# Kernel optimization log

Measured on AMD Instinct MI355X. Metric: run time of the kernel, lower is better.

Reference implementation:

```python
import jax, jax.numpy as jnp
import numpy as np

B, L, D, H, M = 2, 1024, 1024, 16, 64
DH = D // H  # depth per head


def setup_inputs() -> dict:
    key = jax.random.key(0)
    ks = jax.random.split(key, 7)
    s = 0.02
    return {
        "x": jax.random.normal(ks[0], (B, L, D), jnp.float32),
        "Wq": jax.random.normal(ks[1], (D, D), jnp.float32) * s,
        "Wk": jax.random.normal(ks[2], (D, D), jnp.float32) * s,
        "Wv": jax.random.normal(ks[3], (D, D), jnp.float32) * s,
        "Wo": jax.random.normal(ks[4], (D, D), jnp.float32) * s,
        "rel_k_table": jax.random.normal(ks[5], (2 * M + 1, DH), jnp.float32) * s,
        "rel_v_table": jax.random.normal(ks[6], (2 * M + 1, DH), jnp.float32) * s,
    }


def _rel_idx(length, max_rel):
    # Shaw-style clipped relative position indices: [L, L] in [0, 2*max_rel]
    r = jnp.arange(length)
    return jnp.clip(r[None, :] - r[:, None], -max_rel, max_rel) + max_rel


def _split_heads(t):
    # [B, L, D] -> [B, H, L, DH]
    return t.reshape(B, L, H, DH).transpose(0, 2, 1, 3)


def reference(x, Wq, Wk, Wv, Wo, rel_k_table, rel_v_table):
    q = _split_heads(x @ Wq) * (DH ** -0.5)  # T2T scales q by d_head^-0.5
    k = _split_heads(x @ Wk)
    v = _split_heads(x @ Wv)

    idx = _rel_idx(L, M)
    rel_k = rel_k_table[idx]  # [L, L, DH] gathered keys-relative embeddings
    rel_v = rel_v_table[idx]  # [L, L, DH]

    # _relative_attention_inner(q, k, rel_k, transpose=True)
    logits = jnp.einsum('bhid,bhjd->bhij', q, k) + jnp.einsum('bhid,ijd->bhij', q, rel_k)
    w = jax.nn.softmax(logits, axis=-1)  # [B, H, L, L]; dropout_rate=0 / inference

    # _relative_attention_inner(w, v, rel_v, transpose=False)
    o = jnp.einsum('bhij,bhjd->bhid', w, v) + jnp.einsum('bhij,ijd->bhid', w, rel_v)

    # combine heads then output transform
    o = o.transpose(0, 2, 1, 3).reshape(B, L, D)
    return o @ Wo
```

## Files before the change

kernel.cpp:

```cpp
#include <hip/hip_runtime.h>
#include <hip/hip_bf16.h>
#include <math.h>

#define B_ 2
#define L_ 1024
#define D_ 1024
#define H_ 16
#define DH_ 64
#define M_ 64
#define R_ 129
#define NLD ((size_t)B_ * L_ * D_)
#define DD  ((size_t)D_ * D_)
#define QSCALE 0.18033688011112042f

using bf16x8 = __attribute__((ext_vector_type(8))) short;
using f32x4  = __attribute__((ext_vector_type(4))) float;

__device__ __forceinline__ unsigned short f2bf(float f) {
    unsigned int x = __builtin_bit_cast(unsigned int, f);
    unsigned int r = x + 0x7fffu + ((x >> 16) & 1u);
    return (unsigned short)(r >> 16);
}
__device__ __forceinline__ float bf2f(unsigned short u) {
    unsigned int x = ((unsigned int)u) << 16;
    return __builtin_bit_cast(float, x);
}
__device__ __forceinline__ unsigned int pk2bf(float lo, float hi) {
    return (unsigned int)f2bf(lo) | ((unsigned int)f2bf(hi) << 16);
}

__global__ __launch_bounds__(256)
void prep(const float* __restrict__ x,
          const float* __restrict__ W0, const float* __restrict__ W1,
          const float* __restrict__ W2, const float* __restrict__ W3,
          const float* __restrict__ relk, const float* __restrict__ relv,
          unsigned short* __restrict__ xb, unsigned short* __restrict__ Wt,
          unsigned short* __restrict__ relkb, unsigned short* __restrict__ relvT)
{
    __shared__ float tile[32][33];
    const int bid = blockIdx.x, t = threadIdx.x;
    if (bid < 2048) {
        const int i = bid * 256 + t;
        float4 v = ((const float4*)x)[i];
        short4 o = { (short)f2bf(v.x), (short)f2bf(v.y), (short)f2bf(v.z), (short)f2bf(v.w) };
        ((short4*)xb)[i] = o;
    } else if (bid < 6144) {
        const int wb = bid - 2048;
        const int z = wb >> 10, rem = wb & 1023;
        const float* W = z == 0 ? W0 : z == 1 ? W1 : z == 2 ? W2 : W3;
        unsigned short* T = Wt + (size_t)z * DD;
        const int k0 = (rem >> 5) * 32, n0 = (rem & 31) * 32;
        const int r = t >> 3, c = (t & 7) * 4;
        float4 v = *(const float4*)&W[(size_t)(k0 + r) * D_ + n0 + c];
        tile[r][c] = v.x; tile[r][c + 1] = v.y; tile[r][c + 2] = v.z; tile[r][c + 3] = v.w;
        __syncthreads();
        short4 o = { (short)f2bf(tile[c][r]),     (short)f2bf(tile[c + 1][r]),
                     (short)f2bf(tile[c + 2][r]), (short)f2bf(tile[c + 3][r]) };
        *(short4*)&T[(size_t)(n0 + r) * D_ + k0 + c] = o;
    } else {
        const int idx = (bid - 6144) * 256 + t;
        if (idx < 144 * 64) {
            const int r = idx >> 6, d = idx & 63;
            relkb[idx] = (r < R_) ? f2bf(relk[r * 64 + d]) : (unsigned short)0;
        }
        if (idx < 64 * 136) {
            const int d = idx / 136, r = idx - d * 136;
            relvT[idx] = (r < R_) ? f2bf(relv[r * 64 + d]) : (unsigned short)0;
        }
    }
}

__global__ __launch_bounds__(256)
void gemm128(const unsigned short* __restrict__ A, const unsigned short* __restrict__ Bt,
             unsigned short* __restrict__ Cb, float* __restrict__ Cf, float scale0)
{
    __shared__ unsigned short As[128][64];
    __shared__ unsigned short Bs[128][64];

    const int t = threadIdx.x, lane = t & 63, wid = t >> 6;
    const int fr = lane & 15, g = lane >> 4;
    const int m0 = blockIdx.y * 128;
    const int nglob = blockIdx.x * 128;
    const int mat = nglob >> 10;
    const int n0 = nglob & 1023;
    const float scale = (mat == 0) ? scale0 : 1.f;
    const int wm = (wid >> 1) * 64, wn = (wid & 1) * 64;

    f32x4 acc[4][4] = {};

    int srow[4], skof[4], sdst[4];
#pragma unroll
    for (int c = 0; c < 4; ++c) {
        const int chunk = c * 256 + t;
        srow[c] = chunk >> 3;
        skof[c] = ((chunk & 7) ^ (srow[c] & 7)) * 8;
        sdst[c] = chunk * 8;
    }

    const unsigned short* Abase = A  + (size_t)m0 * D_;
    const unsigned short* Bbase = Bt + (size_t)nglob * D_;

    for (int k0 = 0; k0 < D_; k0 += 64) {
        __syncthreads();
#pragma unroll
        for (int c = 0; c < 4; ++c) {
            __builtin_amdgcn_global_load_lds(
                (const __attribute__((address_space(1))) void*)(Abase + (size_t)srow[c] * D_ + k0 + skof[c]),
                (__attribute__((address_space(3))) void*)(&As[0][0] + sdst[c]), 16, 0, 0);
            __builtin_amdgcn_global_load_lds(
                (const __attribute__((address_space(1))) void*)(Bbase + (size_t)srow[c] * D_ + k0 + skof[c]),
                (__attribute__((address_space(3))) void*)(&Bs[0][0] + sdst[c]), 16, 0, 0);
        }
        __syncthreads();

#pragma unroll
        for (int kb = 0; kb < 2; ++kb) {
            bf16x8 av[4], bv[4];
#pragma unroll
            for (int i = 0; i < 4; ++i) {
                const int ra = wm + i * 16 + fr;
                av[i] = *(const bf16x8*)&As[ra][(((kb << 2) + g) ^ (ra & 7)) * 8];
                const int rb = wn + i * 16 + fr;
                bv[i] = *(const bf16x8*)&Bs[rb][(((kb << 2) + g) ^ (rb & 7)) * 8];
            }
#pragma unroll
            for (int i = 0; i < 4; ++i)
#pragma unroll
                for (int j = 0; j < 4; ++j)
                    acc[i][j] = __builtin_amdgcn_mfma_f32_16x16x32_bf16(av[i], bv[j], acc[i][j], 0, 0, 0);
        }
    }

    const int orow = g * 4;
    if (Cb) {
        unsigned short* Cp = Cb + (size_t)mat * NLD;
#pragma unroll
        for (int i = 0; i < 4; ++i)
#pragma unroll
            for (int j = 0; j < 4; ++j) {
                unsigned short* cp = Cp + (size_t)(m0 + wm + i * 16 + orow) * D_ + n0 + wn + j * 16 + fr;
#pragma unroll
                for (int rg = 0; rg < 4; ++rg)
                    cp[(size_t)rg * D_] = f2bf(acc[i][j][rg] * scale);
            }
    } else {
#pragma unroll
        for (int i = 0; i < 4; ++i)
#pragma unroll
            for (int j = 0; j < 4; ++j) {
                float* cp = Cf + (size_t)(m0 + wm + i * 16 + orow) * D_ + n0 + wn + j * 16 + fr;
#pragma unroll
                for (int rg = 0; rg < 4; ++rg)
                    cp[(size_t)rg * D_] = acc[i][j][rg] * scale;
            }
    }
}

__device__ __forceinline__ void stage_k(const unsigned short* src, unsigned short* dst, int t)
{
#pragma unroll
    for (int it = 0; it < 2; ++it) {
        const int c = it * 256 + t;
        const int j = c >> 3;
        const int sc = (c & 7) ^ (j & 7);
        __builtin_amdgcn_global_load_lds(
            (const __attribute__((address_space(1))) void*)(src + (size_t)j * D_ + sc * 8),
            (__attribute__((address_space(3))) void*)(dst + c * 8), 16, 0, 0);
    }
}

__device__ __forceinline__ void write_vt(unsigned short (*Vtl)[64], int jp, int d0, bf16x8 a, bf16x8 b)
{
    const int jlo = (2 * jp) & 7;
    const int jc  = jp >> 2;
#pragma unroll
    for (int e = 0; e < 8; ++e) {
        const int d = d0 + e;
        const unsigned int val = (unsigned int)(unsigned short)a[e]
                               | ((unsigned int)(unsigned short)b[e] << 16);
        *(unsigned int*)&Vtl[d][((jc ^ (d & 7)) << 3) + jlo] = val;
    }
}

__global__ __launch_bounds__(256)
void attn_mfma(const unsigned short* __restrict__ Qb, const unsigned short* __restrict__ Kb,
               const unsigned short* __restrict__ Vb,
               const unsigned short* __restrict__ relkb,
               const unsigned short* __restrict__ relvT,
               const float* __restrict__ relv,
               unsigned short* __restrict__ Ob)
{
    __shared__ unsigned short Klds[2][64][64];
    __shared__ unsigned short Vt[2][64][64];
    __shared__ unsigned short Plds[64][72];
    __shared__ unsigned short QRs[64][136];
    __shared__ unsigned short Wsum[64][136];

    const int t    = threadIdx.x;
    const int lane = t & 63;
    const int w    = t >> 6;
    const int fr   = lane & 15;
    const int g    = lane >> 4;

    const int bx  = blockIdx.x;
    const int xcd = bx & 7, slot = bx >> 3;
    const int bh  = (xcd << 2) | (slot >> 4);
    const int rb  = slot & 15;
    const int b   = bh >> 4, h = bh & 15;
    const int i0  = rb * 64;
    const size_t head = (size_t)b * L_ * D_ + (size_t)h * DH_;

    const int iloc = w * 16 + fr;

    const unsigned short* Kh = Kb + head;
    const unsigned short* Vh = Vb + head;

    stage_k(Kh, &Klds[0][0][0], t);

    const int jp = t & 31, d0v = ((t >> 5) & 7) * 8;
    bf16x8 va  = *(const bf16x8*)(Vh + (size_t)(2 * jp) * D_ + d0v);
    bf16x8 vb2 = *(const bf16x8*)(Vh + (size_t)(2 * jp + 1) * D_ + d0v);

    {
        unsigned int* wp = (unsigned int*)&Wsum[0][0];
        for (int i = t; i < 64 * 136 / 2; i += 256) wp[i] = 0u;
    }

    bf16x8 qf[2];
    {
        const unsigned short* qp = Qb + head + (size_t)(i0 + iloc) * D_;
        qf[0] = *(const bf16x8*)(qp + g * 8);
        qf[1] = *(const bf16x8*)(qp + 32 + g * 8);
    }

#pragma unroll
    for (int rc = 0; rc < 9; ++rc) {
        f32x4 acc = {};
#pragma unroll
        for (int kb = 0; kb < 2; ++kb) {
            bf16x8 rv = *(const bf16x8*)&relkb[(size_t)(rc * 16 + fr) * 64 + kb * 32 + g * 8];
            acc = __builtin_amdgcn_mfma_f32_16x16x32_bf16(rv, qf[kb], acc, 0, 0, 0);
        }
        if (rc < 8) {
            uint2 pk = { pk2bf(acc[0], acc[1]), pk2bf(acc[2], acc[3]) };
            *(uint2*)&QRs[iloc][rc * 16 + g * 4] = pk;
        } else if (g == 0) {
            QRs[iloc][128] = f2bf(acc[0]);
        }
    }

    write_vt(Vt[0], jp, d0v, va, vb2);
    asm volatile("s_waitcnt vmcnt(0)" ::: "memory");
    __syncthreads();

    const float qr0   = bf2f(QRs[iloc][0]);
    const float qr128 = bf2f(QRs[iloc][128]);

    f32x4 oacc[4] = {};
    float lpart = 0.f, pe0p = 0.f, pe128p = 0.f;

    int bb = 0;
    for (int jt = 0; jt < 16; ++jt) {
        const bool pre = (jt < 15);
        if (pre) {
            stage_k(Kh + (size_t)(jt + 1) * 64 * D_, &Klds[bb ^ 1][0][0], t);
            const unsigned short* vp = Vh + (size_t)((jt + 1) * 64 + 2 * jp) * D_ + d0v;
            va  = *(const bf16x8*)vp;
            vb2 = *(const bf16x8*)(vp + D_);
        }

        f32x4 s[4];
        __builtin_amdgcn_s_setprio(1);
#pragma unroll
        for (int fc = 0; fc < 4; ++fc) {
            f32x4 a = {};
            const int j = fc * 16 + fr;
#pragma unroll
            for (int kb = 0; kb < 2; ++kb) {
                bf16x8 kv = *(const bf16x8*)&Klds[bb][j][(((kb << 2) + g) ^ (j & 7)) * 8];
                a = __builtin_amdgcn_mfma_f32_16x16x32_bf16(kv, qf[kb], a, 0, 0, 0);
            }
            s[fc] = a;
        }
        __builtin_amdgcn_s_setprio(0);

        const int dt   = (jt - rb) * 64;
        const int relb = dt - iloc + g * 4;

        if (dt <= -128 || dt >= 128) {
            const float qrc = (dt < 0) ? qr0 : qr128;
            float tsum = 0.f;
#pragma unroll
            for (int fc = 0; fc < 4; ++fc) {
                float p0 = exp2f(s[fc][0] + qrc);
                float p1 = exp2f(s[fc][1] + qrc);
                float p2 = exp2f(s[fc][2] + qrc);
                float p3 = exp2f(s[fc][3] + qrc);
                uint2 pk = { pk2bf(p0, p1), pk2bf(p2, p3) };
                *(uint2*)&Plds[iloc][fc * 16 + g * 4] = pk;
                tsum += (p0 + p1) + (p2 + p3);
            }
            lpart += tsum;
            if (dt < 0) pe0p += tsum; else pe128p += tsum;
        } else if (dt == 0) {
#pragma unroll
            for (int fc = 0; fc < 4; ++fc) {
                const int c0 = relb + fc * 16 + M_;
                float pe[4];
#pragma unroll
                for (int reg = 0; reg < 4; ++reg) {
                    pe[reg] = exp2f(s[fc][reg] + bf2f(QRs[iloc][c0 + reg]));
                    lpart += pe[reg];
                }
                uint2 pk = { pk2bf(pe[0], pe[1]), pk2bf(pe[2], pe[3]) };
                *(uint2*)&Plds[iloc][fc * 16 + g * 4] = pk;
                Wsum[iloc][c0 + 0] = (unsigned short)(pk.x & 0xffffu);
                Wsum[iloc][c0 + 1] = (unsigned short)(pk.x >> 16);
                Wsum[iloc][c0 + 2] = (unsigned short)(pk.y & 0xffffu);
                Wsum[iloc][c0 + 3] = (unsigned short)(pk.y >> 16);
            }
        } else {
#pragma unroll
            for (int fc = 0; fc < 4; ++fc) {
                float pe[4];
#pragma unroll
                for (int reg = 0; reg < 4; ++reg) {
                    const int colr = relb + fc * 16 + reg + M_;
                    const int col  = colr < 0 ? 0 : (colr > 128 ? 128 : colr);
                    pe[reg] = exp2f(s[fc][reg] + bf2f(QRs[iloc][col]));
                    lpart += pe[reg];
                    if (col == 0)        pe0p   += pe[reg];
                    else if (col == 128) pe128p += pe[reg];
                    else                 Wsum[iloc][col] = f2bf(pe[reg]);
                }
                uint2 pk = { pk2bf(pe[0], pe[1]), pk2bf(pe[2], pe[3]) };
                *(uint2*)&Plds[iloc][fc * 16 + g * 4] = pk;
            }
        }

        asm volatile("s_waitcnt lgkmcnt(0)" ::: "memory");
        __builtin_amdgcn_sched_barrier(0);

        bf16x8 pa0 = *(const bf16x8*)&Plds[iloc][g * 8];
        bf16x8 pa1 = *(const bf16x8*)&Plds[iloc][32 + g * 8];
        __builtin_amdgcn_s_setprio(1);
#pragma unroll
        for (int fd = 0; fd < 4; ++fd) {
            const int d = fd * 16 + fr;
            bf16x8 vv0 = *(const bf16x8*)&Vt[bb][d][((g)     ^ (d & 7)) * 8];
            bf16x8 vv1 = *(const bf16x8*)&Vt[bb][d][((4 + g) ^ (d & 7)) * 8];
            oacc[fd] = __builtin_amdgcn_mfma_f32_16x16x32_bf16(pa0, vv0, oacc[fd], 0, 0, 0);
            oacc[fd] = __builtin_amdgcn_mfma_f32_16x16x32_bf16(pa1, vv1, oacc[fd], 0, 0, 0);
        }
        __builtin_amdgcn_s_setprio(0);

        if (pre) write_vt(Vt[bb ^ 1], jp, d0v, va, vb2);
        asm volatile("s_waitcnt vmcnt(0)" ::: "memory");
        __syncthreads();
        bb ^= 1;
    }

    lpart  += __shfl_xor(lpart, 16);  lpart  += __shfl_xor(lpart, 32);
    pe0p   += __shfl_xor(pe0p, 16);   pe0p   += __shfl_xor(pe0p, 32);
    pe128p += __shfl_xor(pe128p, 16); pe128p += __shfl_xor(pe128p, 32);
    if (g == 0) {
        Wsum[iloc][0]   = f2bf(pe0p);
        Wsum[iloc][128] = f2bf(pe128p);
    }
    asm volatile("s_waitcnt lgkmcnt(0)" ::: "memory");
    __builtin_amdgcn_sched_barrier(0);

#pragma unroll
    for (int kc = 0; kc < 4; ++kc) {
        bf16x8 wa = *(const bf16x8*)&Wsum[iloc][kc * 32 + g * 8];
#pragma unroll
        for (int fd = 0; fd < 4; ++fd) {
            bf16x8 rv = *(const bf16x8*)&relvT[(size_t)(fd * 16 + fr) * 136 + kc * 32 + g * 8];
            oacc[fd] = __builtin_amdgcn_mfma_f32_16x16x32_bf16(wa, rv, oacc[fd], 0, 0, 0);
        }
    }

    float invd[4], pr128[4];
#pragma unroll
    for (int reg = 0; reg < 4; ++reg) {
        const int src = (lane & 48) | (g * 4 + reg);
        invd[reg]  = 1.f / __shfl(lpart, src, 64);
        pr128[reg] = __shfl(pe128p, src, 64);
    }

#pragma unroll
    for (int fd = 0; fd < 4; ++fd) {
        const float r128 = relv[128 * 64 + fd * 16 + fr];
        unsigned short* op = Ob + head + (size_t)(i0 + w * 16 + g * 4) * D_ + fd * 16 + fr;
#pragma unroll
        for (int reg = 0; reg < 4; ++reg)
            op[(size_t)reg * D_] = f2bf((oacc[fd][reg] + pr128[reg] * r128) * invd[reg]);
    }
}

extern "C" void kernel_launch(void* const* d_in, const int* in_sizes, int n_in,
                              void* d_out, int out_size, void* d_ws, size_t ws_size,
                              hipStream_t stream)
{
    const float* x    = (const float*)d_in[0];
    const float* Wq   = (const float*)d_in[1];
    const float* Wk   = (const float*)d_in[2];
    const float* Wv   = (const float*)d_in[3];
    const float* Wo   = (const float*)d_in[4];
    const float* relk = (const float*)d_in[5];
    const float* relv = (const float*)d_in[6];
    float* out = (float*)d_out;

    unsigned short* xb    = (unsigned short*)d_ws;
    unsigned short* Wt    = xb + NLD;
    unsigned short* relkb = Wt + 4 * DD;
    unsigned short* relvT = relkb + 144 * 64;
    unsigned short* QKVb  = relvT + 64 * 136;
    unsigned short* Ob    = QKVb + 3 * NLD;

    prep<<<dim3(6180), 256, 0, stream>>>(x, Wq, Wk, Wv, Wo, relk, relv, xb, Wt, relkb, relvT);

    gemm128<<<dim3(24, 16), 256, 0, stream>>>(xb, Wt, QKVb, nullptr, QSCALE);

    attn_mfma<<<dim3(512), 256, 0, stream>>>(QKVb, QKVb + NLD, QKVb + 2 * NLD,
                                             relkb, relvT, relv, Ob);

    gemm128<<<dim3(8, 16), 256, 0, stream>>>(Ob, Wt + 3 * DD, nullptr, out, 1.f);
}
```

Before: 91.63 us.

## Shrink GEMM M-tile to 64, hoist V loads in attention, use intrinsic bf16 pack

The projection GEMMs now use a 64x128 tile, so the QKV GEMM runs 768 blocks and the output GEMM 256 blocks. That gives more parallelism on the many CUs, at the price of less reuse of each B tile. In the attention kernel, the V fragment LDS reads are moved ahead of the softmax section so their latency overlaps the exp work, which costs extra registers. The manual float-to-bf16 pair packing is replaced with the HIP __float22bfloat162_rn intrinsic, which may map to a packed convert instruction.

```diff
diff --git a/kernel.cpp b/kernel.cpp
--- a/kernel.cpp
+++ b/kernel.cpp
@@ -26,7 +26,10 @@
     return __builtin_bit_cast(float, x);
 }
 __device__ __forceinline__ unsigned int pk2bf(float lo, float hi) {
-    return (unsigned int)f2bf(lo) | ((unsigned int)f2bf(hi) << 16);
+    __hip_bfloat162 h = __float22bfloat162_rn(float2{lo, hi});
+    unsigned int u;
+    __builtin_memcpy(&u, &h, 4);
+    return u;
 }
 
 __global__ __launch_bounds__(256)
@@ -71,30 +74,38 @@
 }
 
 __global__ __launch_bounds__(256)
-void gemm128(const unsigned short* __restrict__ A, const unsigned short* __restrict__ Bt,
-             unsigned short* __restrict__ Cb, float* __restrict__ Cf, float scale0)
-{
-    __shared__ unsigned short As[128][64];
+void gemm64(const unsigned short* __restrict__ A, const unsigned short* __restrict__ Bt,
+            unsigned short* __restrict__ Cb, float* __restrict__ Cf, float scale0)
+{
+    __shared__ unsigned short As[64][64];
     __shared__ unsigned short Bs[128][64];
 
     const int t = threadIdx.x, lane = t & 63, wid = t >> 6;
     const int fr = lane & 15, g = lane >> 4;
-    const int m0 = blockIdx.y * 128;
+    const int m0 = blockIdx.y * 64;
     const int nglob = blockIdx.x * 128;
     const int mat = nglob >> 10;
     const int n0 = nglob & 1023;
     const float scale = (mat == 0) ? scale0 : 1.f;
-    const int wm = (wid >> 1) * 64, wn = (wid & 1) * 64;
-
-    f32x4 acc[4][4] = {};
-
-    int srow[4], skof[4], sdst[4];
+    const int wm = (wid >> 1) * 32, wn = (wid & 1) * 64;
+
+    f32x4 acc[2][4] = {};
+
+    int arow[2], akof[2], adst[2];
+#pragma unroll
+    for (int c = 0; c < 2; ++c) {
+        const int chunk = c * 256 + t;
+        arow[c] = chunk >> 3;
+        akof[c] = ((chunk & 7) ^ (arow[c] & 7)) * 8;
+        adst[c] = chunk * 8;
+    }
+    int brow[4], bkof[4], bdst[4];
 #pragma unroll
     for (int c = 0; c < 4; ++c) {
         const int chunk = c * 256 + t;
-        srow[c] = chunk >> 3;
-        skof[c] = ((chunk & 7) ^ (srow[c] & 7)) * 8;
-        sdst[c] = chunk * 8;
+        brow[c] = chunk >> 3;
+        bkof[c] = ((chunk & 7) ^ (brow[c] & 7)) * 8;
+        bdst[c] = chunk * 8;
     }
 
     const unsigned short* Abase = A  + (size_t)m0 * D_;
@@ -103,28 +114,32 @@
     for (int k0 = 0; k0 < D_; k0 += 64) {
         __syncthreads();
 #pragma unroll
-        for (int c = 0; c < 4; ++c) {
+        for (int c = 0; c < 2; ++c)
             __builtin_amdgcn_global_load_lds(
-                (const __attribute__((address_space(1))) void*)(Abase + (size_t)srow[c] * D_ + k0 + skof[c]),
-                (__attribute__((address_space(3))) void*)(&As[0][0] + sdst[c]), 16, 0, 0);
+                (const __attribute__((address_space(1))) void*)(Abase + (size_t)arow[c] * D_ + k0 + akof[c]),
+                (__attribute__((address_space(3))) void*)(&As[0][0] + adst[c]), 16, 0, 0);
+#pragma unroll
+        for (int c = 0; c < 4; ++c)
             __builtin_amdgcn_global_load_lds(
-                (const __attribute__((address_space(1))) void*)(Bbase + (size_t)srow[c] * D_ + k0 + skof[c]),
-                (__attribute__((address_space(3))) void*)(&Bs[0][0] + sdst[c]), 16, 0, 0);
-        }
+                (const __attribute__((address_space(1))) void*)(Bbase + (size_t)brow[c] * D_ + k0 + bkof[c]),
+                (__attribute__((address_space(3))) void*)(&Bs[0][0] + bdst[c]), 16, 0, 0);
         __syncthreads();
 
 #pragma unroll
         for (int kb = 0; kb < 2; ++kb) {
-            bf16x8 av[4], bv[4];
-#pragma unroll
-            for (int i = 0; i < 4; ++i) {
+            bf16x8 av[2], bv[4];
+#pragma unroll
+            for (int i = 0; i < 2; ++i) {
                 const int ra = wm + i * 16 + fr;
                 av[i] = *(const bf16x8*)&As[ra][(((kb << 2) + g) ^ (ra & 7)) * 8];
-                const int rb = wn + i * 16 + fr;
-                bv[i] = *(const bf16x8*)&Bs[rb][(((kb << 2) + g) ^ (rb & 7)) * 8];
-            }
-#pragma unroll
-            for (int i = 0; i < 4; ++i)
+            }
+#pragma unroll
+            for (int j = 0; j < 4; ++j) {
+                const int rb = wn + j * 16 + fr;
+                bv[j] = *(const bf16x8*)&Bs[rb][(((kb << 2) + g) ^ (rb & 7)) * 8];
+            }
+#pragma unroll
+            for (int i = 0; i < 2; ++i)
 #pragma unroll
                 for (int j = 0; j < 4; ++j)
                     acc[i][j] = __builtin_amdgcn_mfma_f32_16x16x32_bf16(av[i], bv[j], acc[i][j], 0, 0, 0);
@@ -135,7 +150,7 @@
     if (Cb) {
         unsigned short* Cp = Cb + (size_t)mat * NLD;
 #pragma unroll
-        for (int i = 0; i < 4; ++i)
+        for (int i = 0; i < 2; ++i)
 #pragma unroll
             for (int j = 0; j < 4; ++j) {
                 unsigned short* cp = Cp + (size_t)(m0 + wm + i * 16 + orow) * D_ + n0 + wn + j * 16 + fr;
@@ -145,7 +160,7 @@
             }
     } else {
 #pragma unroll
-        for (int i = 0; i < 4; ++i)
+        for (int i = 0; i < 2; ++i)
 #pragma unroll
             for (int j = 0; j < 4; ++j) {
                 float* cp = Cf + (size_t)(m0 + wm + i * 16 + orow) * D_ + n0 + wn + j * 16 + fr;
@@ -283,6 +298,14 @@
             s[fc] = a;
         }
         __builtin_amdgcn_s_setprio(0);
+
+        bf16x8 vv0[4], vv1[4];
+#pragma unroll
+        for (int fd = 0; fd < 4; ++fd) {
+            const int d = fd * 16 + fr;
+            vv0[fd] = *(const bf16x8*)&Vt[bb][d][((g)     ^ (d & 7)) * 8];
+            vv1[fd] = *(const bf16x8*)&Vt[bb][d][((4 + g) ^ (d & 7)) * 8];
+        }
 
         const int dt   = (jt - rb) * 64;
         const int relb = dt - iloc + g * 4;
@@ -346,11 +369,8 @@
         __builtin_amdgcn_s_setprio(1);
 #pragma unroll
         for (int fd = 0; fd < 4; ++fd) {
-            const int d = fd * 16 + fr;
-            bf16x8 vv0 = *(const bf16x8*)&Vt[bb][d][((g)     ^ (d & 7)) * 8];
-            bf16x8 vv1 = *(const bf16x8*)&Vt[bb][d][((4 + g) ^ (d & 7)) * 8];
-            oacc[fd] = __builtin_amdgcn_mfma_f32_16x16x32_bf16(pa0, vv0, oacc[fd], 0, 0, 0);
-            oacc[fd] = __builtin_amdgcn_mfma_f32_16x16x32_bf16(pa1, vv1, oacc[fd], 0, 0, 0);
+            oacc[fd] = __builtin_amdgcn_mfma_f32_16x16x32_bf16(pa0, vv0[fd], oacc[fd], 0, 0, 0);
+            oacc[fd] = __builtin_amdgcn_mfma_f32_16x16x32_bf16(pa1, vv1[fd], oacc[fd], 0, 0, 0);
         }
         __builtin_amdgcn_s_setprio(0);
 
@@ -420,10 +440,10 @@
 
     prep<<<dim3(6180), 256, 0, stream>>>(x, Wq, Wk, Wv, Wo, relk, relv, xb, Wt, relkb, relvT);
 
-    gemm128<<<dim3(24, 16), 256, 0, stream>>>(xb, Wt, QKVb, nullptr, QSCALE);
+    gemm64<<<dim3(24, 32), 256, 0, stream>>>(xb, Wt, QKVb, nullptr, QSCALE);
 
     attn_mfma<<<dim3(512), 256, 0, stream>>>(QKVb, QKVb + NLD, QKVb + 2 * NLD,
                                              relkb, relvT, relv, Ob);
 
-    gemm128<<<dim3(8, 16), 256, 0, stream>>>(Ob, Wt + 3 * DD, nullptr, out, 1.f);
-}
+    gemm64<<<dim3(8, 32), 256, 0, stream>>>(Ob, Wt + 3 * DD, nullptr, out, 1.f);
+}
```

Result: faster. 82.44 us (-10.0%).
